# Performance work log

Measured on AMD Instinct MI355X. Metric: run time of the kernel, lower is better.

Reference implementation:

```python
import jax, jax.numpy as jnp
import numpy as np
from jax import lax

D_MODEL, D_STATE, D_CONV, EXPAND = 512, 16, 4, 2
D_INNER = EXPAND * D_MODEL          # 1024
DT_RANK = (D_MODEL + 15) // 16      # 32
BATCH, SEQ = 4, 1024


def setup_inputs() -> dict:
    key = jax.random.key(0)
    ks = jax.random.split(key, 8)
    s = 0.02
    x = jax.random.normal(ks[0], (BATCH, SEQ, D_MODEL), jnp.float32)
    in_proj_w = jax.random.normal(ks[1], (2 * D_INNER, D_MODEL), jnp.float32) * s
    conv_w = jax.random.normal(ks[2], (D_INNER, 1, D_CONV), jnp.float32) * s  # depthwise
    conv_b = jnp.zeros((D_INNER,), jnp.float32)
    x_proj_w = jax.random.normal(ks[3], (DT_RANK + 2 * D_STATE, D_INNER), jnp.float32) * s
    dt_proj_w = jax.random.normal(ks[4], (D_INNER, DT_RANK), jnp.float32) * s
    dt_proj_b = jax.random.normal(ks[5], (D_INNER,), jnp.float32) * 0.1
    # Mamba S4D-real init: A = -[1..d_state] per channel, stored as log
    A_log = jnp.log(jnp.tile(jnp.arange(1, D_STATE + 1, dtype=jnp.float32)[None, :], (D_INNER, 1)))
    D = jnp.ones((D_INNER,), jnp.float32)
    out_proj_w = jax.random.normal(ks[6], (D_MODEL, D_INNER), jnp.float32) * s
    ln_w = jnp.ones((D_MODEL,), jnp.float32)
    ln_b = jnp.zeros((D_MODEL,), jnp.float32)
    return dict(x=x, in_proj_w=in_proj_w, conv_w=conv_w, conv_b=conv_b,
                x_proj_w=x_proj_w, dt_proj_w=dt_proj_w, dt_proj_b=dt_proj_b,
                A_log=A_log, D=D, out_proj_w=out_proj_w, ln_w=ln_w, ln_b=ln_b)


def _selective_scan(u, delta, A, Bm, Cm, D):
    # u, delta: (B,L,Di); A: (Di,N); Bm, Cm: (B,L,N)
    dA = jnp.exp(delta[..., None] * A)                    # (B,L,Di,N)
    dBu = (delta * u)[..., None] * Bm[:, :, None, :]      # (B,L,Di,N)
    dA_t = jnp.moveaxis(dA, 1, 0)                         # (L,B,Di,N)
    dBu_t = jnp.moveaxis(dBu, 1, 0)
    C_t = jnp.moveaxis(Cm, 1, 0)                          # (L,B,N)

    def step(h, inp):
        dA_i, dBu_i, C_i = inp
        h = dA_i * h + dBu_i                              # (B,Di,N)
        y = jnp.einsum('bdn,bn->bd', h, C_i)
        return h, y

    h0 = jnp.zeros((u.shape[0], A.shape[0], A.shape[1]), u.dtype)
    _, ys = lax.scan(step, h0, (dA_t, dBu_t, C_t))        # ys: (L,B,Di)
    return jnp.moveaxis(ys, 0, 1) + u * D                 # (B,L,Di)


def reference(x, in_proj_w, conv_w, conv_b, x_proj_w, dt_proj_w, dt_proj_b,
              A_log, D, out_proj_w, ln_w, ln_b):
    # ---- Mamba SSM ----
    xz = jnp.einsum('bld,ed->ble', x, in_proj_w)          # (B,L,2*Di)
    xs, z = jnp.split(xz, 2, axis=-1)
    # causal depthwise conv over time
    xt = jnp.moveaxis(xs, 1, 2)                           # (B,Di,L)
    xt = lax.conv_general_dilated(xt, conv_w, window_strides=(1,),
                                  padding=[(D_CONV - 1, 0)],
                                  feature_group_count=D_INNER,
                                  dimension_numbers=('NCH', 'OIH', 'NCH'))
    xt = xt + conv_b[None, :, None]
    u = jax.nn.silu(jnp.moveaxis(xt, 1, 2))               # (B,L,Di)

    x_dbl = jnp.einsum('bld,ed->ble', u, x_proj_w)        # (B,L,dt_rank+2N)
    dt = x_dbl[..., :DT_RANK]
    Bm = x_dbl[..., DT_RANK:DT_RANK + D_STATE]
    Cm = x_dbl[..., DT_RANK + D_STATE:]
    delta = jax.nn.softplus(jnp.einsum('blr,dr->bld', dt, dt_proj_w) + dt_proj_b)
    A = -jnp.exp(A_log)                                   # (Di,N)

    y = _selective_scan(u, delta, A, Bm, Cm, D)
    y = y * jax.nn.silu(z)
    ssm_out = jnp.einsum('ble,de->bld', y, out_proj_w)    # (B,L,Dm)

    # ---- residual + LayerNorm ----
    r = x + ssm_out
    mu = jnp.mean(r, axis=-1, keepdims=True)
    var = jnp.mean(jnp.square(r - mu), axis=-1, keepdims=True)
    return (r - mu) / jnp.sqrt(var + 1e-5) * ln_w + ln_b
```

## Files before the change

kernel.cpp:

```cpp
#include <hip/hip_runtime.h>
#include <hip/hip_bf16.h>
#include <math.h>

#define B_   4
#define L_   1024
#define DM   512
#define DI   1024
#define NS   16
#define XDC  64
#define BL   4096
#define G_   16
#define SEG  64
#define KS   4

typedef short bfrag __attribute__((ext_vector_type(8)));
typedef float ffrag __attribute__((ext_vector_type(4)));

__device__ __forceinline__ ushort f2bf(float v) {
    __hip_bfloat16 h = __float2bfloat16(v);
    return *(ushort*)&h;
}

__global__ __launch_bounds__(256) void cast_bf16(const float* __restrict__ in,
        ushort* __restrict__ out, int n4)
{
    int i = blockIdx.x * 256 + threadIdx.x;
    if (i >= n4) return;
    float4 v = ((const float4*)in)[i];
    ushort4 o;
    o.x = f2bf(v.x); o.y = f2bf(v.y); o.z = f2bf(v.z); o.w = f2bf(v.w);
    ((ushort4*)out)[i] = o;
}

template<int EPI>
__global__ __launch_bounds__(256) void gemm_mfma(const ushort* __restrict__ A,
        const ushort* __restrict__ B, float* __restrict__ C,
        int K, int ldc, const float* __restrict__ resid,
        const float* __restrict__ bias)
{
    __shared__ ushort As[128][40];
    __shared__ ushort Bs[128][40];
    const int tid = threadIdx.x;
    const int lane = tid & 63, wave = tid >> 6;
    const int wm = (wave & 1) * 64, wn = (wave >> 1) * 64;
    const int l15 = lane & 15, quad = lane >> 4;
    const int m0 = blockIdx.y * 128, n0 = blockIdx.x * 128;

    ffrag acc[4][4] = {};

    for (int k0 = 0; k0 < K; k0 += 32) {
        #pragma unroll
        for (int i = 0; i < 2; i++) {
            int chunk = tid + i * 256;
            int row = chunk >> 2, kk8 = (chunk & 3) * 8;
            *(uint4*)&As[row][kk8] = *(const uint4*)&A[(size_t)(m0 + row) * K + k0 + kk8];
            *(uint4*)&Bs[row][kk8] = *(const uint4*)&B[(size_t)(n0 + row) * K + k0 + kk8];
        }
        __syncthreads();
        bfrag af[4], bfv[4];
        #pragma unroll
        for (int i = 0; i < 4; i++) {
            af[i]  = *(const bfrag*)&As[wm + i * 16 + l15][quad * 8];
            bfv[i] = *(const bfrag*)&Bs[wn + i * 16 + l15][quad * 8];
        }
        #pragma unroll
        for (int i = 0; i < 4; i++)
            #pragma unroll
            for (int j = 0; j < 4; j++)
                acc[i][j] = __builtin_amdgcn_mfma_f32_16x16x32_bf16(af[i], bfv[j], acc[i][j], 0, 0, 0);
        __syncthreads();
    }

    #pragma unroll
    for (int i = 0; i < 4; i++) {
        #pragma unroll
        for (int j = 0; j < 4; j++) {
            int n = n0 + wn + j * 16 + l15;
            #pragma unroll
            for (int r = 0; r < 4; r++) {
                int m = m0 + wm + i * 16 + quad * 4 + r;
                float v = acc[i][j][r];
                if (EPI == 2) v += resid[(size_t)m * ldc + n];
                if (EPI == 3) {
                    v += bias[m];
                    v = (v > 20.f) ? v : log1pf(__expf(v));
                }
                C[(size_t)m * ldc + n] = v;
            }
        }
    }
}

__global__ __launch_bounds__(256) void gemm3_splitk(const float* __restrict__ uT,
        const float* __restrict__ xw, float* __restrict__ part)
{
    __shared__ float As[16][33];
    __shared__ float Ws[16][68];
    const int tid = threadIdx.x;
    const int tx = tid & 15, ty = tid >> 4;
    const int ks = blockIdx.x, m0 = blockIdx.y * 32;
    const int kbase = ks * (DI / KS);
    float acc[2][4] = {};

    for (int k0 = 0; k0 < DI / KS; k0 += 16) {
        if (tid < 128) {
            int k = tid >> 3, m4 = (tid & 7) * 4;
            const float4 v = *(const float4*)&uT[(size_t)(kbase + k0 + k) * BL + m0 + m4];
            As[k][m4 + 0] = v.x; As[k][m4 + 1] = v.y;
            As[k][m4 + 2] = v.z; As[k][m4 + 3] = v.w;
        }
        {
            int r = tid >> 2, c4 = (tid & 3) * 4;
            const float4 v = *(const float4*)&xw[(size_t)r * DI + kbase + k0 + c4];
            Ws[c4 + 0][r] = v.x; Ws[c4 + 1][r] = v.y;
            Ws[c4 + 2][r] = v.z; Ws[c4 + 3][r] = v.w;
        }
        __syncthreads();
        #pragma unroll
        for (int kk = 0; kk < 16; kk++) {
            float a[2], b[4];
            a[0] = As[kk][ty * 2 + 0];
            a[1] = As[kk][ty * 2 + 1];
            #pragma unroll
            for (int j = 0; j < 4; j++) b[j] = Ws[kk][tx * 4 + j];
            #pragma unroll
            for (int i = 0; i < 2; i++)
                #pragma unroll
                for (int j = 0; j < 4; j++)
                    acc[i][j] = fmaf(a[i], b[j], acc[i][j]);
        }
        __syncthreads();
    }

    float* pp = part + (size_t)ks * BL * XDC;
    #pragma unroll
    for (int i = 0; i < 2; i++) {
        int m = m0 + ty * 2 + i;
        *(float4*)&pp[(size_t)m * XDC + tx * 4] =
            make_float4(acc[i][0], acc[i][1], acc[i][2], acc[i][3]);
    }
}

__global__ __launch_bounds__(256) void gemm3_reduce(const float* __restrict__ part,
        float* __restrict__ xdbl, ushort* __restrict__ dtB)
{
    int i = blockIdx.x * 256 + threadIdx.x;
    const float4* p0 = (const float4*)part;
    float4 a = p0[i];
    #pragma unroll
    for (int s = 1; s < KS; s++) {
        float4 b = p0[i + (size_t)s * BL * XDC / 4];
        a.x += b.x; a.y += b.y; a.z += b.z; a.w += b.w;
    }
    ((float4*)xdbl)[i] = a;
    int c4 = i & 15;
    if (c4 < 8) {
        int m = i >> 4;
        ushort4 o;
        o.x = f2bf(a.x); o.y = f2bf(a.y); o.z = f2bf(a.z); o.w = f2bf(a.w);
        ((ushort4*)dtB)[m * 8 + c4] = o;
    }
}

__global__ __launch_bounds__(256) void conv_silu(const float* __restrict__ xzT,
        const float* __restrict__ cw, const float* __restrict__ cb,
        float* __restrict__ uT)
{
    int i = blockIdx.x * 256 + threadIdx.x;
    int d  = i >> 10;
    int q  = i & 1023;
    int bl = q * 4;
    int l  = bl & (L_ - 1);
    const float* row = xzT + (size_t)d * BL;
    float4 cur = *(const float4*)&row[bl];
    float4 prev = make_float4(0.f, 0.f, 0.f, 0.f);
    if (l != 0) prev = *(const float4*)&row[bl - 4];
    float v[7] = { prev.y, prev.z, prev.w, cur.x, cur.y, cur.z, cur.w };
    float w0 = cw[d * 4 + 0], w1 = cw[d * 4 + 1], w2 = cw[d * 4 + 2], w3 = cw[d * 4 + 3];
    float bias = cb[d];
    float4 o;
    o.x = bias + w0 * v[0] + w1 * v[1] + w2 * v[2] + w3 * v[3];
    o.y = bias + w0 * v[1] + w1 * v[2] + w2 * v[3] + w3 * v[4];
    o.z = bias + w0 * v[2] + w1 * v[3] + w2 * v[4] + w3 * v[5];
    o.w = bias + w0 * v[3] + w1 * v[4] + w2 * v[5] + w3 * v[6];
    o.x = o.x / (1.f + __expf(-o.x));
    o.y = o.y / (1.f + __expf(-o.y));
    o.z = o.z / (1.f + __expf(-o.z));
    o.w = o.w / (1.f + __expf(-o.w));
    *(float4*)&uT[(size_t)d * BL + bl] = o;
}

__global__ __launch_bounds__(256) void scan_fused(const float* __restrict__ deltaT,
        const float* __restrict__ uT, const float* __restrict__ xdbl,
        const float* __restrict__ xzT, const float* __restrict__ A_log,
        const float* __restrict__ Dp, float* __restrict__ yT)
{
    __shared__ float hend_s[G_][NS + 1];
    __shared__ float h0_s[G_][NS + 1];
    __shared__ float sdv_s[G_];

    const int tid = threadIdx.x;
    const int n = tid & 15;
    const int seg = tid >> 4;
    const int bd = blockIdx.x;
    const int d = bd & (DI - 1);
    const int b = bd >> 10;

    const float Acoef = -__expf(A_log[d * NS + n]);
    const float Dd = Dp[d];

    const size_t base_t = (size_t)d * BL + b * L_ + seg * SEG;
    const size_t base_z = (size_t)(DI + d) * BL + b * L_ + seg * SEG;
    const size_t base_x = (size_t)b * L_ * XDC + (size_t)seg * SEG * XDC;

    float h = 0.f, sdv = 0.f;
    for (int l0 = 0; l0 < SEG; l0 += 16) {
        float dv[16], uv[16], Bv[16];
        {
            const float4* dp = (const float4*)(deltaT + base_t + l0);
            const float4* up = (const float4*)(uT + base_t + l0);
            #pragma unroll
            for (int i = 0; i < 4; i++) {
                *(float4*)&dv[i * 4] = dp[i];
                *(float4*)&uv[i * 4] = up[i];
            }
        }
        {
            const float* xp = xdbl + base_x + (size_t)l0 * XDC + 32 + n;
            #pragma unroll
            for (int j = 0; j < 16; j++) Bv[j] = xp[j * XDC];
        }
        #pragma unroll
        for (int j = 0; j < 16; j++) {
            sdv += dv[j];
            Bv[j] *= dv[j] * uv[j];
            dv[j] = __expf(dv[j] * Acoef);
        }
        #pragma unroll
        for (int j = 0; j < 16; j++)
            h = fmaf(dv[j], h, Bv[j]);
    }
    hend_s[seg][n] = h;
    if (n == 0) sdv_s[seg] = sdv;
    __syncthreads();

    if (seg == 0) {
        float H = 0.f;
        #pragma unroll
        for (int s = 0; s < G_; s++) {
            h0_s[s][n] = H;
            H = hend_s[s][n] + __expf(Acoef * sdv_s[s]) * H;
        }
    }
    __syncthreads();

    h = h0_s[seg][n];
    for (int l0 = 0; l0 < SEG; l0 += 16) {
        float ug = uT [base_t + l0 + n];
        float zg = xzT[base_z + l0 + n];

        float dv[16], uv[16];
        {
            const float4* dp = (const float4*)(deltaT + base_t + l0);
            const float4* up = (const float4*)(uT + base_t + l0);
            #pragma unroll
            for (int i = 0; i < 4; i++) {
                *(float4*)&dv[i * 4] = dp[i];
                *(float4*)&uv[i * 4] = up[i];
            }
        }
        float Bv[16], Cv[16];
        {
            const float* xp = xdbl + base_x + (size_t)l0 * XDC + 32 + n;
            #pragma unroll
            for (int j = 0; j < 16; j++) {
                Bv[j] = xp[j * XDC];
                Cv[j] = xp[j * XDC + 16];
            }
        }
        #pragma unroll
        for (int j = 0; j < 16; j++) {
            Bv[j] *= dv[j] * uv[j];
            dv[j] = __expf(dv[j] * Acoef);
        }
        float p[16];
        #pragma unroll
        for (int j = 0; j < 16; j++) {
            h = fmaf(dv[j], h, Bv[j]);
            p[j] = h * Cv[j];
        }

        float q8[8];
        #pragma unroll
        for (int k = 0; k < 8; k++) {
            float tt = (n & 8) ? p[k] : p[k + 8];
            float rr = __shfl_xor(tt, 8);
            q8[k] = ((n & 8) ? p[k + 8] : p[k]) + rr;
        }
        float q4[4];
        #pragma unroll
        for (int k = 0; k < 4; k++) {
            float tt = (n & 4) ? q8[k] : q8[k + 4];
            float rr = __shfl_xor(tt, 4);
            q4[k] = ((n & 4) ? q8[k + 4] : q8[k]) + rr;
        }
        float q2[2];
        #pragma unroll
        for (int k = 0; k < 2; k++) {
            float tt = (n & 2) ? q4[k] : q4[k + 2];
            float rr = __shfl_xor(tt, 2);
            q2[k] = ((n & 2) ? q4[k + 2] : q4[k]) + rr;
        }
        float tt = (n & 1) ? q2[0] : q2[1];
        float rr = __shfl_xor(tt, 1);
        float S = ((n & 1) ? q2[1] : q2[0]) + rr;

        float v = S + ug * Dd;
        v *= zg / (1.f + __expf(-zg));
        yT[base_t + l0 + n] = v;
    }
}

__global__ __launch_bounds__(256) void transpose_cast(const float* __restrict__ yT,
        ushort* __restrict__ yB)
{
    __shared__ float t[64][65];
    const int bl0 = blockIdx.x * 64, d0 = blockIdx.y * 64;
    const int tid = threadIdx.x;
    #pragma unroll
    for (int i = 0; i < 4; i++) {
        int chunk = tid + i * 256;
        int dr = chunk >> 4, c4 = (chunk & 15) * 4;
        const float4 v = *(const float4*)&yT[(size_t)(d0 + dr) * BL + bl0 + c4];
        t[dr][c4 + 0] = v.x; t[dr][c4 + 1] = v.y;
        t[dr][c4 + 2] = v.z; t[dr][c4 + 3] = v.w;
    }
    __syncthreads();
    #pragma unroll
    for (int i = 0; i < 4; i++) {
        int chunk = tid + i * 256;
        int br = chunk >> 4, dc4 = (chunk & 15) * 4;
        ushort4 o;
        o.x = f2bf(t[dc4 + 0][br]); o.y = f2bf(t[dc4 + 1][br]);
        o.z = f2bf(t[dc4 + 2][br]); o.w = f2bf(t[dc4 + 3][br]);
        *(ushort4*)&yB[(size_t)(bl0 + br) * DI + d0 + dc4] = o;
    }
}

__global__ __launch_bounds__(256) void ln_kernel(const float* __restrict__ r,
        const float* __restrict__ lnw, const float* __restrict__ lnb,
        float* __restrict__ out)
{
    int row = blockIdx.x;
    const float* rr = r + (size_t)row * DM;
    float v0 = rr[threadIdx.x], v1 = rr[threadIdx.x + 256];
    float s = v0 + v1, s2 = v0 * v0 + v1 * v1;
    #pragma unroll
    for (int off = 32; off > 0; off >>= 1) {
        s  += __shfl_down(s, off);
        s2 += __shfl_down(s2, off);
    }
    __shared__ float ls[4], ls2[4];
    __shared__ float mu_s, rstd_s;
    int wid = threadIdx.x >> 6, lane = threadIdx.x & 63;
    if (lane == 0) { ls[wid] = s; ls2[wid] = s2; }
    __syncthreads();
    if (threadIdx.x == 0) {
        float S = ls[0] + ls[1] + ls[2] + ls[3];
        float S2 = ls2[0] + ls2[1] + ls2[2] + ls2[3];
        float mu = S * (1.f / DM);
        float var = S2 * (1.f / DM) - mu * mu;
        mu_s = mu;
        rstd_s = rsqrtf(var + 1e-5f);
    }
    __syncthreads();
    float mu = mu_s, rstd = rstd_s;
    out[(size_t)row * DM + threadIdx.x] =
        (v0 - mu) * rstd * lnw[threadIdx.x] + lnb[threadIdx.x];
    out[(size_t)row * DM + threadIdx.x + 256] =
        (v1 - mu) * rstd * lnw[threadIdx.x + 256] + lnb[threadIdx.x + 256];
}

extern "C" void kernel_launch(void* const* d_in, const int* in_sizes, int n_in,
                              void* d_out, int out_size, void* d_ws, size_t ws_size,
                              hipStream_t stream)
{
    const float* x         = (const float*)d_in[0];
    const float* in_proj_w = (const float*)d_in[1];
    const float* conv_w    = (const float*)d_in[2];
    const float* conv_b    = (const float*)d_in[3];
    const float* x_proj_w  = (const float*)d_in[4];
    const float* dt_proj_w = (const float*)d_in[5];
    const float* dt_proj_b = (const float*)d_in[6];
    const float* A_log     = (const float*)d_in[7];
    const float* Dvec      = (const float*)d_in[8];
    const float* out_proj_w= (const float*)d_in[9];
    const float* ln_w      = (const float*)d_in[10];
    const float* ln_b      = (const float*)d_in[11];
    float* out = (float*)d_out;

    float* ws     = (float*)d_ws;
    float* xzT    = ws;
    float* uT     = xzT    + (size_t)2048 * BL;
    float* xdbl   = uT     + (size_t)DI * BL;
    float* deltaT = xdbl   + (size_t)BL * XDC;
    float* yT     = deltaT + (size_t)DI * BL;
    float* r      = yT     + (size_t)DI * BL;
    ushort* xB    = (ushort*)yT;
    float*  xdblp = yT;
    ushort* yB    = (ushort*)deltaT;
    ushort* wOutB = (ushort*)deltaT + (size_t)4 * 1024 * 1024;
    ushort* wInB  = (ushort*)deltaT + (size_t)9 * 1024 * 1024 / 2;
    ushort* dtB   = (ushort*)r;
    ushort* dtwB  = (ushort*)r + (size_t)BL * 32;

    dim3 blk(256);

    cast_bf16<<<(BL * DM / 4 + 255) / 256, blk, 0, stream>>>(x, xB, BL * DM / 4);
    cast_bf16<<<(2048 * DM / 4 + 255) / 256, blk, 0, stream>>>(in_proj_w, wInB, 2048 * DM / 4);
    cast_bf16<<<(DI * 32 / 4 + 255) / 256, blk, 0, stream>>>(dt_proj_w, dtwB, DI * 32 / 4);

    gemm_mfma<0><<<dim3(BL / 128, 2048 / 128), blk, 0, stream>>>(
        wInB, xB, xzT, DM, BL, nullptr, nullptr);

    conv_silu<<<(DI * BL / 4) / 256, blk, 0, stream>>>(xzT, conv_w, conv_b, uT);

    gemm3_splitk<<<dim3(KS, BL / 32), blk, 0, stream>>>(uT, x_proj_w, xdblp);
    gemm3_reduce<<<(BL * XDC / 4) / 256, blk, 0, stream>>>(xdblp, xdbl, dtB);

    gemm_mfma<3><<<dim3(BL / 128, DI / 128), blk, 0, stream>>>(
        dtwB, dtB, deltaT, 32, BL, nullptr, dt_proj_b);

    scan_fused<<<B_ * DI, blk, 0, stream>>>(
        deltaT, uT, xdbl, xzT, A_log, Dvec, yT);

    transpose_cast<<<dim3(BL / 64, DI / 64), blk, 0, stream>>>(yT, yB);
    cast_bf16<<<(DM * DI / 4 + 255) / 256, blk, 0, stream>>>(out_proj_w, wOutB, DM * DI / 4);

    gemm_mfma<2><<<dim3(DM / 128, BL / 128), blk, 0, stream>>>(
        yB, wOutB, r, DI, DM, x, nullptr);

    ln_kernel<<<BL, blk, 0, stream>>>(r, ln_w, ln_b, out);
}
```

Measured before the change: 269.5 us.

## Transpose B/C to state-major layout, fuse casts, use exp2 in scan

The x_proj reduction now writes B and C into separate (batch, state, length) arrays, so the scan loads them with contiguous float4 reads instead of strided scalar gathers. The four bf16 cast launches are merged into one kernel, and the scan uses exp2f with a log2e-prescaled A coefficient. Workspace buffers are rearranged to fit the new arrays, which means the wOutB cast now runs early and its buffer must not be overwritten before the final GEMM.

```diff
diff --git a/kernel.cpp b/kernel.cpp
--- a/kernel.cpp
+++ b/kernel.cpp
@@ -12,6 +12,7 @@
 #define G_   16
 #define SEG  64
 #define KS   4
+#define LOG2E 1.44269504f
 
 typedef short bfrag __attribute__((ext_vector_type(8)));
 typedef float ffrag __attribute__((ext_vector_type(4)));
@@ -21,15 +22,23 @@
     return *(ushort*)&h;
 }
 
-__global__ __launch_bounds__(256) void cast_bf16(const float* __restrict__ in,
-        ushort* __restrict__ out, int n4)
+__global__ __launch_bounds__(256) void cast_all(const float* __restrict__ x,
+        const float* __restrict__ ipw, const float* __restrict__ dtw,
+        const float* __restrict__ opw, ushort* __restrict__ xB,
+        ushort* __restrict__ wInB, ushort* __restrict__ dtwB,
+        ushort* __restrict__ wOutB)
 {
     int i = blockIdx.x * 256 + threadIdx.x;
-    if (i >= n4) return;
-    float4 v = ((const float4*)in)[i];
+    const float4* src; ushort4* dst; int idx;
+    if (i < 524288)      { src = (const float4*)x;   dst = (ushort4*)xB;    idx = i; }
+    else if (i < 786432) { src = (const float4*)ipw; dst = (ushort4*)wInB;  idx = i - 524288; }
+    else if (i < 794624) { src = (const float4*)dtw; dst = (ushort4*)dtwB;  idx = i - 786432; }
+    else if (i < 925696) { src = (const float4*)opw; dst = (ushort4*)wOutB; idx = i - 794624; }
+    else return;
+    float4 v = src[idx];
     ushort4 o;
     o.x = f2bf(v.x); o.y = f2bf(v.y); o.z = f2bf(v.z); o.w = f2bf(v.w);
-    ((ushort4*)out)[i] = o;
+    dst[idx] = o;
 }
 
 template<int EPI>
@@ -142,7 +151,7 @@
 }
 
 __global__ __launch_bounds__(256) void gemm3_reduce(const float* __restrict__ part,
-        float* __restrict__ xdbl, ushort* __restrict__ dtB)
+        ushort* __restrict__ dtB, float* __restrict__ Bsc, float* __restrict__ Csc)
 {
     int i = blockIdx.x * 256 + threadIdx.x;
     const float4* p0 = (const float4*)part;
@@ -152,13 +161,21 @@
         float4 b = p0[i + (size_t)s * BL * XDC / 4];
         a.x += b.x; a.y += b.y; a.z += b.z; a.w += b.w;
     }
-    ((float4*)xdbl)[i] = a;
     int c4 = i & 15;
+    int m = i >> 4;
     if (c4 < 8) {
-        int m = i >> 4;
         ushort4 o;
         o.x = f2bf(a.x); o.y = f2bf(a.y); o.z = f2bf(a.z); o.w = f2bf(a.w);
         ((ushort4*)dtB)[m * 8 + c4] = o;
+    } else {
+        int b = m >> 10, l = m & (L_ - 1);
+        float* dst;
+        int nb;
+        if (c4 < 12) { nb = (c4 - 8) * 4;  dst = Bsc; }
+        else         { nb = (c4 - 12) * 4; dst = Csc; }
+        dst += ((size_t)(b * NS + nb)) * L_ + l;
+        dst[0 * L_] = a.x; dst[1 * L_] = a.y;
+        dst[2 * L_] = a.z; dst[3 * L_] = a.w;
     }
 }
 
@@ -191,9 +208,10 @@
 }
 
 __global__ __launch_bounds__(256) void scan_fused(const float* __restrict__ deltaT,
-        const float* __restrict__ uT, const float* __restrict__ xdbl,
-        const float* __restrict__ xzT, const float* __restrict__ A_log,
-        const float* __restrict__ Dp, float* __restrict__ yT)
+        const float* __restrict__ uT, const float* __restrict__ Bsc,
+        const float* __restrict__ Csc, const float* __restrict__ xzT,
+        const float* __restrict__ A_log, const float* __restrict__ Dp,
+        float* __restrict__ yT)
 {
     __shared__ float hend_s[G_][NS + 1];
     __shared__ float h0_s[G_][NS + 1];
@@ -206,12 +224,12 @@
     const int d = bd & (DI - 1);
     const int b = bd >> 10;
 
-    const float Acoef = -__expf(A_log[d * NS + n]);
+    const float Acoef = -__expf(A_log[d * NS + n]) * LOG2E;
     const float Dd = Dp[d];
 
-    const size_t base_t = (size_t)d * BL + b * L_ + seg * SEG;
-    const size_t base_z = (size_t)(DI + d) * BL + b * L_ + seg * SEG;
-    const size_t base_x = (size_t)b * L_ * XDC + (size_t)seg * SEG * XDC;
+    const size_t base_t  = (size_t)d * BL + b * L_ + seg * SEG;
+    const size_t base_z  = (size_t)(DI + d) * BL + b * L_ + seg * SEG;
+    const size_t base_bc = (size_t)(b * NS + n) * L_ + seg * SEG;
 
     float h = 0.f, sdv = 0.f;
     for (int l0 = 0; l0 < SEG; l0 += 16) {
@@ -219,22 +237,19 @@
         {
             const float4* dp = (const float4*)(deltaT + base_t + l0);
             const float4* up = (const float4*)(uT + base_t + l0);
+            const float4* bp = (const float4*)(Bsc + base_bc + l0);
             #pragma unroll
             for (int i = 0; i < 4; i++) {
                 *(float4*)&dv[i * 4] = dp[i];
                 *(float4*)&uv[i * 4] = up[i];
+                *(float4*)&Bv[i * 4] = bp[i];
             }
-        }
-        {
-            const float* xp = xdbl + base_x + (size_t)l0 * XDC + 32 + n;
-            #pragma unroll
-            for (int j = 0; j < 16; j++) Bv[j] = xp[j * XDC];
         }
         #pragma unroll
         for (int j = 0; j < 16; j++) {
             sdv += dv[j];
             Bv[j] *= dv[j] * uv[j];
-            dv[j] = __expf(dv[j] * Acoef);
+            dv[j] = exp2f(dv[j] * Acoef);
         }
         #pragma unroll
         for (int j = 0; j < 16; j++)
@@ -249,7 +264,7 @@
         #pragma unroll
         for (int s = 0; s < G_; s++) {
             h0_s[s][n] = H;
-            H = hend_s[s][n] + __expf(Acoef * sdv_s[s]) * H;
+            H = hend_s[s][n] + exp2f(Acoef * sdv_s[s]) * H;
         }
     }
     __syncthreads();
@@ -259,29 +274,24 @@
         float ug = uT [base_t + l0 + n];
         float zg = xzT[base_z + l0 + n];
 
-        float dv[16], uv[16];
+        float dv[16], uv[16], Bv[16], Cv[16];
         {
             const float4* dp = (const float4*)(deltaT + base_t + l0);
             const float4* up = (const float4*)(uT + base_t + l0);
+            const float4* bp = (const float4*)(Bsc + base_bc + l0);
+            const float4* cp = (const float4*)(Csc + base_bc + l0);
             #pragma unroll
             for (int i = 0; i < 4; i++) {
                 *(float4*)&dv[i * 4] = dp[i];
                 *(float4*)&uv[i * 4] = up[i];
-            }
-        }
-        float Bv[16], Cv[16];
-        {
-            const float* xp = xdbl + base_x + (size_t)l0 * XDC + 32 + n;
-            #pragma unroll
-            for (int j = 0; j < 16; j++) {
-                Bv[j] = xp[j * XDC];
-                Cv[j] = xp[j * XDC + 16];
+                *(float4*)&Bv[i * 4] = bp[i];
+                *(float4*)&Cv[i * 4] = cp[i];
             }
         }
         #pragma unroll
         for (int j = 0; j < 16; j++) {
             Bv[j] *= dv[j] * uv[j];
-            dv[j] = __expf(dv[j] * Acoef);
+            dv[j] = exp2f(dv[j] * Acoef);
         }
         float p[16];
         #pragma unroll
@@ -402,23 +412,23 @@
     float* ws     = (float*)d_ws;
     float* xzT    = ws;
     float* uT     = xzT    + (size_t)2048 * BL;
-    float* xdbl   = uT     + (size_t)DI * BL;
-    float* deltaT = xdbl   + (size_t)BL * XDC;
+    float* deltaT = uT     + (size_t)DI * BL;
     float* yT     = deltaT + (size_t)DI * BL;
     float* r      = yT     + (size_t)DI * BL;
+    float* Bsc    = r      + (size_t)BL * DM;
+    float* Csc    = Bsc    + (size_t)B_ * NS * L_;
+    ushort* wOutB = (ushort*)(Csc + (size_t)B_ * NS * L_);
     ushort* xB    = (ushort*)yT;
     float*  xdblp = yT;
+    ushort* wInB  = (ushort*)deltaT;
     ushort* yB    = (ushort*)deltaT;
-    ushort* wOutB = (ushort*)deltaT + (size_t)4 * 1024 * 1024;
-    ushort* wInB  = (ushort*)deltaT + (size_t)9 * 1024 * 1024 / 2;
     ushort* dtB   = (ushort*)r;
-    ushort* dtwB  = (ushort*)r + (size_t)BL * 32;
+    ushort* dtwB  = dtB + (size_t)BL * 32;
 
     dim3 blk(256);
 
-    cast_bf16<<<(BL * DM / 4 + 255) / 256, blk, 0, stream>>>(x, xB, BL * DM / 4);
-    cast_bf16<<<(2048 * DM / 4 + 255) / 256, blk, 0, stream>>>(in_proj_w, wInB, 2048 * DM / 4);
-    cast_bf16<<<(DI * 32 / 4 + 255) / 256, blk, 0, stream>>>(dt_proj_w, dtwB, DI * 32 / 4);
+    cast_all<<<(925696 + 255) / 256, blk, 0, stream>>>(
+        x, in_proj_w, dt_proj_w, out_proj_w, xB, wInB, dtwB, wOutB);
 
     gemm_mfma<0><<<dim3(BL / 128, 2048 / 128), blk, 0, stream>>>(
         wInB, xB, xzT, DM, BL, nullptr, nullptr);
@@ -426,16 +436,15 @@
     conv_silu<<<(DI * BL / 4) / 256, blk, 0, stream>>>(xzT, conv_w, conv_b, uT);
 
     gemm3_splitk<<<dim3(KS, BL / 32), blk, 0, stream>>>(uT, x_proj_w, xdblp);
-    gemm3_reduce<<<(BL * XDC / 4) / 256, blk, 0, stream>>>(xdblp, xdbl, dtB);
+    gemm3_reduce<<<(BL * XDC / 4) / 256, blk, 0, stream>>>(xdblp, dtB, Bsc, Csc);
 
     gemm_mfma<3><<<dim3(BL / 128, DI / 128), blk, 0, stream>>>(
         dtwB, dtB, deltaT, 32, BL, nullptr, dt_proj_b);
 
     scan_fused<<<B_ * DI, blk, 0, stream>>>(
-        deltaT, uT, xdbl, xzT, A_log, Dvec, yT);
+        deltaT, uT, Bsc, Csc, xzT, A_log, Dvec, yT);
 
     transpose_cast<<<dim3(BL / 64, DI / 64), blk, 0, stream>>>(yT, yB);
-    cast_bf16<<<(DM * DI / 4 + 255) / 256, blk, 0, stream>>>(out_proj_w, wOutB, DM * DI / 4);
 
     gemm_mfma<2><<<dim3(DM / 128, BL / 128), blk, 0, stream>>>(
         yB, wOutB, r, DI, DM, x, nullptr);
```

New measurement: 346.3 us. 28.5% more time.

## Merge weight/input casts into one kernel and compute delta in FP32 directly

Applied to the files above, without the earlier changes.

Folds the three bf16 cast launches (x, in_proj_w, out_proj_w) into a single cast_all kernel and drops the dt_proj weight cast. Replaces the bf16 MFMA GEMM for the dt projection, which had K=32, with a plain FP32 per-thread dot-product kernel that applies bias and softplus. This also removes the bf16 dt copy written in the reduce step and reshuffles the workspace buffers. The aim is fewer launches and less overhead on a small-K GEMM. The cost is scalar FMAs in place of MFMA, plus redundant weight loads per thread, though those should hit cache.

```diff
diff --git a/kernel.cpp b/kernel.cpp
--- a/kernel.cpp
+++ b/kernel.cpp
@@ -21,22 +21,27 @@
     return *(ushort*)&h;
 }
 
-__global__ __launch_bounds__(256) void cast_bf16(const float* __restrict__ in,
-        ushort* __restrict__ out, int n4)
+__global__ __launch_bounds__(256) void cast_all(const float* __restrict__ x,
+        const float* __restrict__ ipw, const float* __restrict__ opw,
+        ushort* __restrict__ xB, ushort* __restrict__ wInB,
+        ushort* __restrict__ wOutB)
 {
     int i = blockIdx.x * 256 + threadIdx.x;
-    if (i >= n4) return;
-    float4 v = ((const float4*)in)[i];
+    const float4* src; ushort4* dst; int idx;
+    if (i < 524288)      { src = (const float4*)x;   dst = (ushort4*)xB;    idx = i; }
+    else if (i < 786432) { src = (const float4*)ipw; dst = (ushort4*)wInB;  idx = i - 524288; }
+    else if (i < 917504) { src = (const float4*)opw; dst = (ushort4*)wOutB; idx = i - 786432; }
+    else return;
+    float4 v = src[idx];
     ushort4 o;
     o.x = f2bf(v.x); o.y = f2bf(v.y); o.z = f2bf(v.z); o.w = f2bf(v.w);
-    ((ushort4*)out)[i] = o;
+    dst[idx] = o;
 }
 
 template<int EPI>
 __global__ __launch_bounds__(256) void gemm_mfma(const ushort* __restrict__ A,
         const ushort* __restrict__ B, float* __restrict__ C,
-        int K, int ldc, const float* __restrict__ resid,
-        const float* __restrict__ bias)
+        int K, int ldc, const float* __restrict__ resid)
 {
     __shared__ ushort As[128][40];
     __shared__ ushort Bs[128][40];
@@ -81,10 +86,6 @@
                 int m = m0 + wm + i * 16 + quad * 4 + r;
                 float v = acc[i][j][r];
                 if (EPI == 2) v += resid[(size_t)m * ldc + n];
-                if (EPI == 3) {
-                    v += bias[m];
-                    v = (v > 20.f) ? v : log1pf(__expf(v));
-                }
                 C[(size_t)m * ldc + n] = v;
             }
         }
@@ -142,7 +143,7 @@
 }
 
 __global__ __launch_bounds__(256) void gemm3_reduce(const float* __restrict__ part,
-        float* __restrict__ xdbl, ushort* __restrict__ dtB)
+        float* __restrict__ xdbl)
 {
     int i = blockIdx.x * 256 + threadIdx.x;
     const float4* p0 = (const float4*)part;
@@ -153,12 +154,28 @@
         a.x += b.x; a.y += b.y; a.z += b.z; a.w += b.w;
     }
     ((float4*)xdbl)[i] = a;
-    int c4 = i & 15;
-    if (c4 < 8) {
-        int m = i >> 4;
-        ushort4 o;
-        o.x = f2bf(a.x); o.y = f2bf(a.y); o.z = f2bf(a.z); o.w = f2bf(a.w);
-        ((ushort4*)dtB)[m * 8 + c4] = o;
+}
+
+__global__ __launch_bounds__(256) void delta_kernel(const float* __restrict__ xdbl,
+        const float* __restrict__ dtw, const float* __restrict__ bias,
+        float* __restrict__ deltaT)
+{
+    int idx = blockIdx.x * 256 + threadIdx.x;
+    int bl = idx & (BL - 1);
+    int dg = idx >> 12;
+    float a[32];
+    const float4* ap = (const float4*)(xdbl + (size_t)bl * XDC);
+    #pragma unroll
+    for (int i = 0; i < 8; i++) *(float4*)&a[i * 4] = ap[i];
+    #pragma unroll
+    for (int r = 0; r < 4; r++) {
+        int d = dg * 4 + r;
+        const float* w = dtw + (size_t)d * 32;
+        float acc = bias[d];
+        #pragma unroll
+        for (int k = 0; k < 32; k++) acc = fmaf(a[k], w[k], acc);
+        acc = (acc > 20.f) ? acc : log1pf(__expf(acc));
+        deltaT[(size_t)d * BL + bl] = acc;
     }
 }
 
@@ -406,39 +423,35 @@
     float* deltaT = xdbl   + (size_t)BL * XDC;
     float* yT     = deltaT + (size_t)DI * BL;
     float* r      = yT     + (size_t)DI * BL;
+    ushort* wOutB = (ushort*)(r + (size_t)BL * DM);
     ushort* xB    = (ushort*)yT;
     float*  xdblp = yT;
+    ushort* wInB  = (ushort*)deltaT;
     ushort* yB    = (ushort*)deltaT;
-    ushort* wOutB = (ushort*)deltaT + (size_t)4 * 1024 * 1024;
-    ushort* wInB  = (ushort*)deltaT + (size_t)9 * 1024 * 1024 / 2;
-    ushort* dtB   = (ushort*)r;
-    ushort* dtwB  = (ushort*)r + (size_t)BL * 32;
 
     dim3 blk(256);
 
-    cast_bf16<<<(BL * DM / 4 + 255) / 256, blk, 0, stream>>>(x, xB, BL * DM / 4);
-    cast_bf16<<<(2048 * DM / 4 + 255) / 256, blk, 0, stream>>>(in_proj_w, wInB, 2048 * DM / 4);
-    cast_bf16<<<(DI * 32 / 4 + 255) / 256, blk, 0, stream>>>(dt_proj_w, dtwB, DI * 32 / 4);
+    cast_all<<<(917504 + 255) / 256, blk, 0, stream>>>(
+        x, in_proj_w, out_proj_w, xB, wInB, wOutB);
 
     gemm_mfma<0><<<dim3(BL / 128, 2048 / 128), blk, 0, stream>>>(
-        wInB, xB, xzT, DM, BL, nullptr, nullptr);
+        wInB, xB, xzT, DM, BL, nullptr);
 
     conv_silu<<<(DI * BL / 4) / 256, blk, 0, stream>>>(xzT, conv_w, conv_b, uT);
 
     gemm3_splitk<<<dim3(KS, BL / 32), blk, 0, stream>>>(uT, x_proj_w, xdblp);
-    gemm3_reduce<<<(BL * XDC / 4) / 256, blk, 0, stream>>>(xdblp, xdbl, dtB);
-
-    gemm_mfma<3><<<dim3(BL / 128, DI / 128), blk, 0, stream>>>(
-        dtwB, dtB, deltaT, 32, BL, nullptr, dt_proj_b);
+    gemm3_reduce<<<(BL * XDC / 4) / 256, blk, 0, stream>>>(xdblp, xdbl);
+
+    delta_kernel<<<(DI / 4 * BL) / 256, blk, 0, stream>>>(
+        xdbl, dt_proj_w, dt_proj_b, deltaT);
 
     scan_fused<<<B_ * DI, blk, 0, stream>>>(
         deltaT, uT, xdbl, xzT, A_log, Dvec, yT);
 
     transpose_cast<<<dim3(BL / 64, DI / 64), blk, 0, stream>>>(yT, yB);
-    cast_bf16<<<(DM * DI / 4 + 255) / 256, blk, 0, stream>>>(out_proj_w, wOutB, DM * DI / 4);
 
     gemm_mfma<2><<<dim3(DM / 128, BL / 128), blk, 0, stream>>>(
-        yB, wOutB, r, DI, DM, x, nullptr);
+        yB, wOutB, r, DI, DM, x);
 
     ln_kernel<<<BL, blk, 0, stream>>>(r, ln_w, ln_b, out);
 }
```

Measured after the change: 271.4 us. About the same (+0.7%).
